# Performance work log

Measured on AMD Instinct MI355X. Metric: run time of the kernel, lower is better.

The kernel has to match this reference:

```python
import jax, jax.numpy as jnp
import numpy as np

N_USERS = 100_000
N_ITEMS = 100_000
D = 64            # args.in_size == args.out_size (GraphConv has weight=None)
N_INTENTS = 128   # hardcoded in DCCF
HID = 128         # SemanticAttention hidden_size
N_UI_EDGES = 1_000_000
N_MP_EDGES = 500_000
N_MP = 2          # metapaths per node type
B = 4096
N_LAYERS = 2      # hardcoded in DCCF


def setup_inputs() -> dict:
    key = jax.random.key(0)
    ks = jax.random.split(key, 20)
    s = 0.1
    inp = {}
    inp['user_feat'] = jax.random.normal(ks[0], (N_USERS, D), jnp.float32) * s
    inp['item_feat'] = jax.random.normal(ks[1], (N_ITEMS, D), jnp.float32) * s
    inp['user_intent'] = jax.random.normal(ks[2], (D, N_INTENTS), jnp.float32) * s
    inp['item_intent'] = jax.random.normal(ks[3], (D, N_INTENTS), jnp.float32) * s
    inp['sa_u_W1'] = jax.random.normal(ks[4], (D, HID), jnp.float32) * s
    inp['sa_u_b1'] = jnp.zeros((HID,), jnp.float32)
    inp['sa_u_w2'] = jax.random.normal(ks[5], (HID,), jnp.float32) * s
    inp['sa_i_W1'] = jax.random.normal(ks[6], (D, HID), jnp.float32) * s
    inp['sa_i_b1'] = jnp.zeros((HID,), jnp.float32)
    inp['sa_i_w2'] = jax.random.normal(ks[7], (HID,), jnp.float32) * s
    inp['ui_src'] = jax.random.randint(ks[8], (N_UI_EDGES,), 0, N_USERS)
    inp['ui_dst'] = jax.random.randint(ks[9], (N_UI_EDGES,), 0, N_ITEMS)
    inp['mp_user'] = jax.random.randint(ks[10], (N_MP, 2, N_MP_EDGES), 0, N_USERS)
    inp['mp_item'] = jax.random.randint(ks[11], (N_MP, 2, N_MP_EDGES), 0, N_ITEMS)
    # indices drawn WITHOUT replacement so torch.unique(index) in ssl_loss is a no-op
    inp['user_idx'] = jax.random.choice(ks[12], N_USERS, (B,), replace=False)
    inp['item_idx'] = jax.random.choice(ks[13], N_ITEMS, (B,), replace=False)
    inp['neg_item_idx'] = jax.random.randint(ks[14], (B,), 0, N_ITEMS)
    return inp


def _forward(user_feat, item_feat, user_intent, item_intent,
             sa_u_W1, sa_u_b1, sa_u_w2, sa_i_W1, sa_i_b1, sa_i_w2,
             ui_src, ui_dst, mp_user, mp_item, user_idx, item_idx, neg_item_idx):
    n_nodes = N_USERS + N_ITEMS
    # symmetric bipartite adjacency in COO (tmp_adj + tmp_adj.T)
    rows = jnp.concatenate([ui_src, ui_dst + N_USERS])
    cols = jnp.concatenate([ui_dst + N_USERS, ui_src])
    deg = jnp.maximum(jax.ops.segment_sum(jnp.ones_like(rows, jnp.float32), rows,
                                          num_segments=n_nodes), 1.0)
    dinv = jax.lax.rsqrt(deg)
    gv = dinv[rows] * dinv[cols]  # G = D^{-1/2} A D^{-1/2}

    def spmm(x):  # gather-scale-scatter, the torch_sparse.spmm
        return jax.ops.segment_sum(gv[:, None] * x[cols], rows, num_segments=n_nodes)

    # ---- DCCF ----
    emb = jnp.concatenate([user_feat, item_feat], axis=0)
    total = emb
    for _ in range(N_LAYERS):
        gnn = spmm(emb)
        u, it = emb[:N_USERS], emb[N_USERS:]
        u_int = jax.nn.softmax(u @ user_intent, axis=1) @ user_intent.T
        i_int = jax.nn.softmax(it @ item_intent, axis=1) @ item_intent.T
        emb = gnn + jnp.concatenate([u_int, i_int], axis=0) + emb
        total = total + emb  # torch.stack(...).sum(dim=1)
    ua, ia = total[:N_USERS], total[N_USERS:]

    # ---- HANLayer: GraphConv(norm='both', weight=None) per metapath ----
    def graphconv(src, dst, h, n):
        ones = jnp.ones_like(src, jnp.float32)
        outdeg = jnp.maximum(jax.ops.segment_sum(ones, src, num_segments=n), 1.0)
        indeg = jnp.maximum(jax.ops.segment_sum(ones, dst, num_segments=n), 1.0)
        x = h * jax.lax.rsqrt(outdeg)[:, None]
        agg = jax.ops.segment_sum(x[src], dst, num_segments=n)
        return agg * jax.lax.rsqrt(indeg)[:, None]

    def sem_att(z, W1, b1, w2):  # z: [N, M, D]
        w = jnp.mean(jnp.tanh(z @ W1 + b1) @ w2, axis=0)  # [M]
        beta = jax.nn.softmax(w)
        return jnp.einsum('m,nmd->nd', beta, z)

    zu = jnp.stack([graphconv(mp_user[m, 0], mp_user[m, 1], user_feat, N_USERS)
                    for m in range(N_MP)], axis=1)
    h2_u = sem_att(zu, sa_u_W1, sa_u_b1, sa_u_w2)
    zi = jnp.stack([graphconv(mp_item[m, 0], mp_item[m, 1], item_feat, N_ITEMS)
                    for m in range(N_MP)], axis=1)
    h2_i = sem_att(zi, sa_i_W1, sa_i_b1, sa_i_w2)

    user_emb = 0.5 * ua + 0.5 * h2_u
    item_emb = 0.5 * ia + 0.5 * h2_i

    def ssl(d1, d2, idx):  # InfoNCE with temp 0.5 (idx already unique)
        e1 = d1[idx]
        e2 = d2[idx]
        e1 = e1 / jnp.linalg.norm(e1, axis=1, keepdims=True)
        e2 = e2 / jnp.linalg.norm(e2, axis=1, keepdims=True)
        pos = jnp.sum(e1 * e2, axis=1) / 0.5
        lse = jax.nn.logsumexp(e1 @ e2.T / 0.5, axis=1)
        return -jnp.sum(pos - lse) / idx.shape[0]

    ssl_loss = ssl(h2_u, ua, user_idx) + ssl(h2_i, ia, item_idx)
    return (user_emb[user_idx], item_emb[item_idx], item_emb[neg_item_idx], ssl_loss)


def reference(user_feat, item_feat, user_intent, item_intent,
              sa_u_W1, sa_u_b1, sa_u_w2, sa_i_W1, sa_i_b1, sa_i_w2,
              ui_src, ui_dst, mp_user, mp_item, user_idx, item_idx, neg_item_idx):
    return _forward(user_feat, item_feat, user_intent, item_intent,
                    sa_u_W1, sa_u_b1, sa_u_w2, sa_i_W1, sa_i_b1, sa_i_w2,
                    ui_src, ui_dst, mp_user, mp_item, user_idx, item_idx, neg_item_idx)
```

## Files before the change

### kernel.cpp

```cpp
#include <hip/hip_runtime.h>
#include <math.h>

#define NUSERS   100000
#define NITEMS   100000
#define NNODES   200000
#define DD       64
#define NI       128
#define E_UI     1000000
#define E_MP     500000
#define BB       4096
#define NSTRIP   6250

#define O_CNT       0LL
#define O_OUTCNT    600000LL
#define O_CURSOR    1000000LL
#define O_PARTIALS  1600000LL
#define O_UITB_U    1625600LL
#define O_UITB_I    1629696LL
#define O_UIB_U     1633792LL
#define O_UIB_I     1637888LL
#define O_W1B_U     1641984LL
#define O_W1B_I     1646080LL
#define O_SUMEXP    1700000LL
#define O_POS       1708192LL
#define ZEND        1716384LL
#define O_OFF       1716384LL
#define O_BSUM      2316448LL
#define O_DINV      2317472LL
#define O_OINV      2517472LL
#define O_IINV      2917472LL
#define O_ADJ       3317472LL
#define O_WSUM      7317472LL
#define O_EMBA      7317480LL
#define O_TOTAL     20117480LL
#define O_EMBB      32917480LL
#define O_E1U       45717480LL
#define O_E2U       45979624LL
#define O_E1I       46241768LL
#define O_E2I       46503912LL

typedef __attribute__((ext_vector_type(8))) short short8;
typedef __attribute__((ext_vector_type(4))) float f32x4;

__device__ __forceinline__ short f2bf(float x) {
  unsigned u = __float_as_uint(x);
  unsigned r = (u + 0x7FFFu + ((u >> 16) & 1u)) >> 16;
  return (short)r;
}

__global__ void k_hist_main(const int* __restrict__ src, const int* __restrict__ dst,
                            int* __restrict__ cnt) {
  int e = blockIdx.x * 256 + threadIdx.x;
  if (e < E_UI) {
    atomicAdd(&cnt[src[e]], 1);
    atomicAdd(&cnt[NUSERS + dst[e]], 1);
  }
}

__global__ void k_hist_mp(const int* __restrict__ mpu, const int* __restrict__ mpi,
                          int* __restrict__ cnt, int* __restrict__ outcnt) {
  int e = blockIdx.x * 256 + threadIdx.x;
  int g = blockIdx.y;
  if (e < E_MP) {
    const int* base = (g < 2) ? (mpu + (long long)g * 2 * E_MP)
                              : (mpi + (long long)(g - 2) * 2 * E_MP);
    int s = base[e];
    int d = base[E_MP + e];
    atomicAdd(&outcnt[g * NUSERS + s], 1);
    atomicAdd(&cnt[NNODES + g * NUSERS + d], 1);
  }
}

__global__ __launch_bounds__(1024) void k_scan1(const int* __restrict__ in, int* __restrict__ out,
                                                int* __restrict__ bsum, int n) {
  __shared__ int s[1024];
  int i = blockIdx.x * 1024 + threadIdx.x;
  int v = (i < n) ? in[i] : 0;
  s[threadIdx.x] = v;
  __syncthreads();
  for (int off = 1; off < 1024; off <<= 1) {
    int x = (threadIdx.x >= off) ? s[threadIdx.x - off] : 0;
    __syncthreads();
    s[threadIdx.x] += x;
    __syncthreads();
  }
  if (i < n) out[i] = s[threadIdx.x] - v;
  if (threadIdx.x == 1023) bsum[blockIdx.x] = s[1023];
}

__global__ __launch_bounds__(1024) void k_scan2(int* __restrict__ bsum, int nb) {
  __shared__ int s[1024];
  int v = (threadIdx.x < nb) ? bsum[threadIdx.x] : 0;
  s[threadIdx.x] = v;
  __syncthreads();
  for (int off = 1; off < 1024; off <<= 1) {
    int x = (threadIdx.x >= off) ? s[threadIdx.x - off] : 0;
    __syncthreads();
    s[threadIdx.x] += x;
    __syncthreads();
  }
  if (threadIdx.x < nb) bsum[threadIdx.x] = s[threadIdx.x] - v;
}

__global__ __launch_bounds__(1024) void k_scan3(int* __restrict__ out, const int* __restrict__ bsum, int n) {
  int i = blockIdx.x * 1024 + threadIdx.x;
  if (i < n) out[i] += bsum[blockIdx.x];
}

__global__ void k_inv(const int* __restrict__ cnt, const int* __restrict__ outcnt,
                      float* __restrict__ dinv, float* __restrict__ iinv, float* __restrict__ oinv) {
  int i = blockIdx.x * 256 + threadIdx.x;
  if (i < NNODES) {
    int c = cnt[i]; if (c < 1) c = 1;
    dinv[i] = 1.0f / sqrtf((float)c);
  } else if (i < 600000) {
    int c = cnt[i]; if (c < 1) c = 1;
    iinv[i - NNODES] = 1.0f / sqrtf((float)c);
  }
  if (i < 400000) {
    int c = outcnt[i]; if (c < 1) c = 1;
    oinv[i] = 1.0f / sqrtf((float)c);
  }
}

__global__ void k_scatter_main(const int* __restrict__ src, const int* __restrict__ dst,
                               const int* __restrict__ off, int* __restrict__ cursor,
                               int* __restrict__ adj) {
  int e = blockIdx.x * 256 + threadIdx.x;
  if (e < E_UI) {
    int u = src[e];
    int it = NUSERS + dst[e];
    int p = atomicAdd(&cursor[u], 1);
    adj[off[u] + p] = it;
    int q = atomicAdd(&cursor[it], 1);
    adj[off[it] + q] = u;
  }
}

__global__ void k_scatter_mp(const int* __restrict__ mpu, const int* __restrict__ mpi,
                             const int* __restrict__ off, int* __restrict__ cursor,
                             int* __restrict__ adj) {
  int e = blockIdx.x * 256 + threadIdx.x;
  int g = blockIdx.y;
  if (e < E_MP) {
    const int* base = (g < 2) ? (mpu + (long long)g * 2 * E_MP)
                              : (mpi + (long long)(g - 2) * 2 * E_MP);
    int s = base[e];
    int d = base[E_MP + e];
    int node = NNODES + g * NUSERS + d;
    int p = atomicAdd(&cursor[node], 1);
    adj[off[node] + p] = s;
  }
}

__global__ void k_init(const float4* __restrict__ uf, const float4* __restrict__ itf,
                       float4* __restrict__ emb) {
  int i = blockIdx.x * 256 + threadIdx.x;
  if (i < 3200000) {
    emb[i] = (i < 1600000) ? uf[i] : itf[i - 1600000];
  }
}

__global__ void k_tw(const float* __restrict__ UIu, const float* __restrict__ UIi,
                     const float* __restrict__ W1u, const float* __restrict__ W1i,
                     short* __restrict__ UITBu, short* __restrict__ UITBi,
                     short* __restrict__ UIBu,  short* __restrict__ UIBi,
                     short* __restrict__ W1Bu,  short* __restrict__ W1Bi) {
  int t = blockIdx.x * 256 + threadIdx.x;
  if (t < 8192) {
    int d = t >> 7, j = t & 127;
    UITBu[j * 64 + d] = f2bf(UIu[t]);
    UITBi[j * 64 + d] = f2bf(UIi[t]);
    UIBu[t] = f2bf(UIu[t]);
    UIBi[t] = f2bf(UIi[t]);
    W1Bu[j * 64 + d] = f2bf(W1u[t]);
    W1Bi[j * 64 + d] = f2bf(W1i[t]);
  }
}

__device__ __forceinline__ float gather_rows(const float* __restrict__ tbl,
                                             const int* __restrict__ adj,
                                             int start, int c,
                                             const float* __restrict__ warr, int wofs,
                                             int lane) {
  float acc = 0.0f;
  for (int kb = 0; kb < c; kb += 64) {
    int rem = c - kb; if (rem > 64) rem = 64;
    int mi = 0; float mw = 0.0f;
    if (lane < rem) { mi = adj[start + kb + lane]; mw = warr[wofs + mi]; }
    for (int k = 0; k < rem; k += 8) {
      int n0=__shfl(mi,k+0),n1=__shfl(mi,k+1),n2=__shfl(mi,k+2),n3=__shfl(mi,k+3);
      int n4=__shfl(mi,k+4),n5=__shfl(mi,k+5),n6=__shfl(mi,k+6),n7=__shfl(mi,k+7);
      float w0=__shfl(mw,k+0),w1=__shfl(mw,k+1),w2=__shfl(mw,k+2),w3=__shfl(mw,k+3);
      float w4=__shfl(mw,k+4),w5=__shfl(mw,k+5),w6=__shfl(mw,k+6),w7=__shfl(mw,k+7);
      float v0=tbl[((long long)n0<<6)+lane], v1=tbl[((long long)n1<<6)+lane];
      float v2=tbl[((long long)n2<<6)+lane], v3=tbl[((long long)n3<<6)+lane];
      float v4=tbl[((long long)n4<<6)+lane], v5=tbl[((long long)n5<<6)+lane];
      float v6=tbl[((long long)n6<<6)+lane], v7=tbl[((long long)n7<<6)+lane];
      acc += w0*v0; acc += w1*v1; acc += w2*v2; acc += w3*v3;
      acc += w4*v4; acc += w5*v5; acc += w6*v6; acc += w7*v7;
    }
  }
  return acc;
}

__global__ __launch_bounds__(256) void k_layer(
    const float* __restrict__ ecur, float* __restrict__ enext, float* __restrict__ total,
    const int* __restrict__ adj, const int* __restrict__ off, const int* __restrict__ cnt,
    const float* __restrict__ dinv,
    const short* __restrict__ UITBu, const short* __restrict__ UITBi,
    const short* __restrict__ UIBu,  const short* __restrict__ UIBi, int layer) {
  __shared__ float sZ[4][16 * 68];
  __shared__ float sP[4][16 * 132];
  int w = threadIdx.x >> 6, lane = threadIdx.x & 63;
  int nb = blockIdx.x * 64 + w * 16;
  const short* UITB = (nb < NUSERS) ? UITBu : UITBi;
  const short* UIB  = (nb < NUSERS) ? UIBu  : UIBi;
  float* rowZ = sZ[w];
  float* rowP = sP[w];

  for (int m = 0; m < 16; m++) {
    int node = nb + m;
    float acc = gather_rows(ecur, adj, off[node], cnt[node], dinv, 0, lane);
    rowZ[m * 68 + lane] = dinv[node] * acc;
  }

  int quad = lane >> 4, mrow = lane & 15;
  const float* vrow = ecur + (((long long)(nb + mrow)) << 6) + quad * 8;
  float4 va0 = *(const float4*)(vrow);
  float4 va1 = *(const float4*)(vrow + 4);
  float4 vc0 = *(const float4*)(vrow + 32);
  float4 vc1 = *(const float4*)(vrow + 36);
  short8 a0 = { f2bf(va0.x), f2bf(va0.y), f2bf(va0.z), f2bf(va0.w),
                f2bf(va1.x), f2bf(va1.y), f2bf(va1.z), f2bf(va1.w) };
  short8 a1 = { f2bf(vc0.x), f2bf(vc0.y), f2bf(vc0.z), f2bf(vc0.w),
                f2bf(vc1.x), f2bf(vc1.y), f2bf(vc1.z), f2bf(vc1.w) };
  float den0 = 0.f, den1 = 0.f, den2 = 0.f, den3 = 0.f;
  float* pw = rowP + (quad * 4) * 132 + mrow;
#pragma unroll
  for (int jt = 0; jt < 8; jt++) {
    const short* wr = UITB + ((jt * 16 + mrow) << 6) + quad * 8;
    short8 b0 = *(const short8*)(wr);
    short8 bh = *(const short8*)(wr + 32);
    f32x4 acc = {0.f, 0.f, 0.f, 0.f};
    acc = __builtin_amdgcn_mfma_f32_16x16x32_bf16(a0, b0, acc, 0, 0, 0);
    acc = __builtin_amdgcn_mfma_f32_16x16x32_bf16(a1, bh, acc, 0, 0, 0);
    float e0 = __expf(acc[0]), e1 = __expf(acc[1]);
    float e2 = __expf(acc[2]), e3 = __expf(acc[3]);
    den0 += e0; den1 += e1; den2 += e2; den3 += e3;
    float* pj = pw + jt * 16;
    pj[0] = e0; pj[132] = e1; pj[264] = e2; pj[396] = e3;
  }
  for (int mask = 1; mask <= 8; mask <<= 1) {
    den0 += __shfl_xor(den0, mask); den1 += __shfl_xor(den1, mask);
    den2 += __shfl_xor(den2, mask); den3 += __shfl_xor(den3, mask);
  }
  float rd0 = 1.f / den0, rd1 = 1.f / den1, rd2 = 1.f / den2, rd3 = 1.f / den3;

#pragma unroll
  for (int dt = 0; dt < 4; dt++) {
    f32x4 acc = {0.f, 0.f, 0.f, 0.f};
#pragma unroll
    for (int c = 0; c < 4; c++) {
      const float* pr = rowP + mrow * 132 + c * 32 + quad * 8;
      float4 p0 = *(const float4*)(pr);
      float4 p1 = *(const float4*)(pr + 4);
      short8 af = { f2bf(p0.x), f2bf(p0.y), f2bf(p0.z), f2bf(p0.w),
                    f2bf(p1.x), f2bf(p1.y), f2bf(p1.z), f2bf(p1.w) };
      const short* br = UIB + ((dt * 16 + mrow) << 7) + c * 32 + quad * 8;
      short8 bf = *(const short8*)(br);
      acc = __builtin_amdgcn_mfma_f32_16x16x32_bf16(af, bf, acc, 0, 0, 0);
    }
    int d = dt * 16 + mrow;
#define COMB(r, rd)                                                            \
    { int node = nb + quad * 4 + r;                                            \
      long long base = (((long long)node) << 6) + d;                           \
      float o = acc[r] * rd;                                                   \
      float gn = rowZ[(quad * 4 + r) * 68 + d];                                \
      float vv = ecur[base];                                                   \
      float ne = gn + o + vv;                                                  \
      enext[base] = ne;                                                        \
      total[base] = (layer == 0) ? (vv + ne) : (total[base] + ne); }
    COMB(0, rd0) COMB(1, rd1) COMB(2, rd2) COMB(3, rd3)
#undef COMB
  }
}

__global__ __launch_bounds__(256, 6) void k_mp_gather(
    const float* __restrict__ uf, const float* __restrict__ itf,
    const int* __restrict__ adj, const int* __restrict__ off, const int* __restrict__ cnt,
    const float* __restrict__ oinv, const float* __restrict__ iinv,
    float* __restrict__ zu, float* __restrict__ zi) {
  int g = blockIdx.y;
  const float* feat = (g < 2) ? uf : itf;
  float* zb = (g < 2) ? zu + ((long long)g * NUSERS << 6)
                      : zi + ((long long)(g - 2) * NUSERS << 6);
  int n = (blockIdx.x << 2) + (threadIdx.x >> 6);
  int lane = threadIdx.x & 63;
  int gofs = g * NUSERS;
  int node = NNODES + gofs + n;
  float z = gather_rows(feat, adj, off[node], cnt[node], oinv, gofs, lane);
  zb[((long long)n << 6) + lane] = z * iinv[gofs + n];
}

__global__ __launch_bounds__(256, 4) void k_mp_mlp(
    const float* __restrict__ zu, const float* __restrict__ zi,
    const short* __restrict__ W1Bu, const float* __restrict__ b1u, const float* __restrict__ w2u,
    const short* __restrict__ W1Bi, const float* __restrict__ b1i, const float* __restrict__ w2i,
    float* __restrict__ partials) {
  int g = blockIdx.y;
  const short* W1B = (g < 2) ? W1Bu : W1Bi;
  const float* b1  = (g < 2) ? b1u : b1i;
  const float* w2  = (g < 2) ? w2u : w2i;
  const float* zb  = (g < 2) ? zu + ((long long)g * NUSERS << 6)
                             : zi + ((long long)(g - 2) * NUSERS << 6);
  int w = threadIdx.x >> 6, lane = threadIdx.x & 63;
  int strip = blockIdx.x * 4 + w;
  if (strip >= NSTRIP) return;
  int quad = lane >> 4, mrow = lane & 15;
  const float* zrow = zb + (((long long)(strip * 16 + mrow)) << 6) + quad * 8;
  float4 za0 = *(const float4*)(zrow);
  float4 za1 = *(const float4*)(zrow + 4);
  float4 zc0 = *(const float4*)(zrow + 32);
  float4 zc1 = *(const float4*)(zrow + 36);
  short8 a0 = { f2bf(za0.x), f2bf(za0.y), f2bf(za0.z), f2bf(za0.w),
                f2bf(za1.x), f2bf(za1.y), f2bf(za1.z), f2bf(za1.w) };
  short8 a1 = { f2bf(zc0.x), f2bf(zc0.y), f2bf(zc0.z), f2bf(zc0.w),
                f2bf(zc1.x), f2bf(zc1.y), f2bf(zc1.z), f2bf(zc1.w) };
  float psum = 0.0f;
#pragma unroll
  for (int jt = 0; jt < 8; jt++) {
    const short* wr = W1B + ((jt * 16 + mrow) << 6) + quad * 8;
    short8 b0 = *(const short8*)(wr);
    short8 bh = *(const short8*)(wr + 32);
    f32x4 acc = {0.f, 0.f, 0.f, 0.f};
    acc = __builtin_amdgcn_mfma_f32_16x16x32_bf16(a0, b0, acc, 0, 0, 0);
    acc = __builtin_amdgcn_mfma_f32_16x16x32_bf16(a1, bh, acc, 0, 0, 0);
    int j = jt * 16 + mrow;
    float bj = b1[j], wj = w2[j];
#pragma unroll
    for (int r = 0; r < 4; r++) {
      float s = acc[r] + bj;
      psum += wj * (1.0f - 2.0f / (__expf(2.0f * s) + 1.0f));
    }
  }
  for (int m = 32; m; m >>= 1) psum += __shfl_xor(psum, m);
  if (lane == 0) partials[g * NSTRIP + strip] = psum;
}

__global__ void k_beta(const float* __restrict__ partials, float* __restrict__ wsum) {
  int g = blockIdx.x;
  float s = 0.0f;
  for (int i = threadIdx.x; i < NSTRIP; i += 256) s += partials[g * NSTRIP + i];
  for (int m = 32; m; m >>= 1) s += __shfl_xor(s, m);
  __shared__ float r[4];
  if ((threadIdx.x & 63) == 0) r[threadIdx.x >> 6] = s;
  __syncthreads();
  if (threadIdx.x == 0) wsum[g] = r[0] + r[1] + r[2] + r[3];
}

__global__ __launch_bounds__(256) void k_h2out(
    const float* __restrict__ zu, const float* __restrict__ zi,
    const int* __restrict__ user_idx, const int* __restrict__ item_idx, const int* __restrict__ neg_idx,
    const float* __restrict__ total,
    const float* __restrict__ wsum, float* __restrict__ out,
    float* __restrict__ e1u, float* __restrict__ e2u,
    float* __restrict__ e1i, float* __restrict__ e2i, float* __restrict__ pos) {
  int lane = threadIdx.x & 63;
  int row = (blockIdx.x << 2) + (threadIdx.x >> 6);
  int seg = row >> 12;
  int r = row & 4095;
  int idx;
  const float* zb;
  int gbase;
  if (seg == 0)      { idx = user_idx[r]; zb = zu; gbase = 0; }
  else if (seg == 1) { idx = item_idx[r]; zb = zi; gbase = 2; }
  else               { idx = neg_idx[r];  zb = zi; gbase = 2; }
  int tnode = gbase ? (NUSERS + idx) : idx;
  float t = total[((long long)tnode << 6) + lane];
  float w0 = wsum[gbase] * (1.0f / 100000.0f);
  float w1 = wsum[gbase + 1] * (1.0f / 100000.0f);
  float mb = fmaxf(w0, w1);
  float b0 = expf(w0 - mb), b1 = expf(w1 - mb);
  float bs = b0 + b1;
  b0 /= bs; b1 /= bs;
  float z0 = zb[((long long)idx << 6) + lane];
  float z1 = zb[(((long long)NUSERS + idx) << 6) + lane];
  float h2 = b0 * z0 + b1 * z1;
  out[((long long)row << 6) + lane] = 0.5f * t + 0.5f * h2;
  if (seg < 2) {
    float n1 = h2 * h2, n2 = t * t;
    for (int m = 32; m; m >>= 1) { n1 += __shfl_xor(n1, m); n2 += __shfl_xor(n2, m); }
    n1 = sqrtf(n1); n2 = sqrtf(n2);
    float a = h2 / n1, b = t / n2;
    float d = a * b;
    for (int m = 32; m; m >>= 1) d += __shfl_xor(d, m);
    float* e1 = seg ? e1i : e1u;
    float* e2 = seg ? e2i : e2u;
    e1[((long long)r << 6) + lane] = a;
    e2[((long long)r << 6) + lane] = b;
    if (lane == 0) pos[seg * BB + r] = 2.0f * d;
  }
}

__global__ __launch_bounds__(256) void k_gemm(const float* __restrict__ e1u, const float* __restrict__ e2u,
                                              const float* __restrict__ e1i, const float* __restrict__ e2i,
                                              float* __restrict__ sumexp) {
  int side = blockIdx.z;
  const float* A = side ? e1i : e1u;
  const float* Bm = side ? e2i : e2u;
  __shared__ float sA[64][68], sB[64][68];
  int bb = blockIdx.y, kk = blockIdx.x;
  int tid = threadIdx.x;
  for (int i = tid; i < 1024; i += 256) {
    int row = i >> 4, d4 = (i & 15) << 2;
    float4 a = *(const float4*)&A[(((long long)(bb * 64 + row)) << 6) + d4];
    float4 b = *(const float4*)&Bm[(((long long)(kk * 64 + row)) << 6) + d4];
    *(float4*)&sA[row][d4] = a;
    *(float4*)&sB[row][d4] = b;
  }
  __syncthreads();
  int tx = tid & 15, ty = tid >> 4;
  int r0 = ty << 2, c0 = tx << 2;
  float acc[4][4] = {{0}};
  for (int k = 0; k < 64; k += 4) {
    float4 a0 = *(const float4*)&sA[r0 + 0][k];
    float4 a1 = *(const float4*)&sA[r0 + 1][k];
    float4 a2 = *(const float4*)&sA[r0 + 2][k];
    float4 a3 = *(const float4*)&sA[r0 + 3][k];
    float4 b0 = *(const float4*)&sB[c0 + 0][k];
    float4 b1 = *(const float4*)&sB[c0 + 1][k];
    float4 b2 = *(const float4*)&sB[c0 + 2][k];
    float4 b3 = *(const float4*)&sB[c0 + 3][k];
#define DOT(u_, v_) (u_.x*v_.x + u_.y*v_.y + u_.z*v_.z + u_.w*v_.w)
    acc[0][0] += DOT(a0, b0); acc[0][1] += DOT(a0, b1); acc[0][2] += DOT(a0, b2); acc[0][3] += DOT(a0, b3);
    acc[1][0] += DOT(a1, b0); acc[1][1] += DOT(a1, b1); acc[1][2] += DOT(a1, b2); acc[1][3] += DOT(a1, b3);
    acc[2][0] += DOT(a2, b0); acc[2][1] += DOT(a2, b1); acc[2][2] += DOT(a2, b2); acc[2][3] += DOT(a2, b3);
    acc[3][0] += DOT(a3, b0); acc[3][1] += DOT(a3, b1); acc[3][2] += DOT(a3, b2); acc[3][3] += DOT(a3, b3);
#undef DOT
  }
#pragma unroll
  for (int i = 0; i < 4; i++) {
    float rs = __expf(2.0f * acc[i][0]) + __expf(2.0f * acc[i][1])
             + __expf(2.0f * acc[i][2]) + __expf(2.0f * acc[i][3]);
    for (int m = 1; m < 16; m <<= 1) rs += __shfl_xor(rs, m);
    if (tx == 0)
      __hip_atomic_fetch_add(&sumexp[side * BB + bb * 64 + r0 + i], rs,
                             __ATOMIC_RELAXED, __HIP_MEMORY_SCOPE_AGENT);
  }
}

__global__ void k_loss(const float* __restrict__ sumexp, const float* __restrict__ pos,
                       float* __restrict__ out) {
  float s = 0.0f;
  for (int i = threadIdx.x; i < 2 * BB; i += 256) s += logf(sumexp[i]) - pos[i];
  for (int m = 32; m; m >>= 1) s += __shfl_xor(s, m);
  __shared__ float r[4];
  if ((threadIdx.x & 63) == 0) r[threadIdx.x >> 6] = s;
  __syncthreads();
  if (threadIdx.x == 0) out[3 * BB * DD] = (r[0] + r[1] + r[2] + r[3]) * (1.0f / (float)BB);
}

extern "C" void kernel_launch(void* const* d_in, const int* in_sizes, int n_in,
                              void* d_out, int out_size, void* d_ws, size_t ws_size,
                              hipStream_t stream) {
  const float* uf  = (const float*)d_in[0];
  const float* itf = (const float*)d_in[1];
  const float* UIu = (const float*)d_in[2];
  const float* UIi = (const float*)d_in[3];
  const float* W1u = (const float*)d_in[4];
  const float* b1u = (const float*)d_in[5];
  const float* w2u = (const float*)d_in[6];
  const float* W1i = (const float*)d_in[7];
  const float* b1i = (const float*)d_in[8];
  const float* w2i = (const float*)d_in[9];
  const int* ui_src   = (const int*)d_in[10];
  const int* ui_dst   = (const int*)d_in[11];
  const int* mpu      = (const int*)d_in[12];
  const int* mpi      = (const int*)d_in[13];
  const int* user_idx = (const int*)d_in[14];
  const int* item_idx = (const int*)d_in[15];
  const int* neg_idx  = (const int*)d_in[16];
  float* out = (float*)d_out;

  float* wf = (float*)d_ws;
  int*   wi = (int*)d_ws;

  int*   cnt      = wi + O_CNT;
  int*   outcnt   = wi + O_OUTCNT;
  int*   cursor   = wi + O_CURSOR;
  float* partials = wf + O_PARTIALS;
  short* UITBu    = (short*)(wf + O_UITB_U);
  short* UITBi    = (short*)(wf + O_UITB_I);
  short* UIBu     = (short*)(wf + O_UIB_U);
  short* UIBi     = (short*)(wf + O_UIB_I);
  short* W1Bu     = (short*)(wf + O_W1B_U);
  short* W1Bi     = (short*)(wf + O_W1B_I);
  float* sumexp   = wf + O_SUMEXP;
  float* pos      = wf + O_POS;
  int*   off      = wi + O_OFF;
  int*   bsum     = wi + O_BSUM;
  float* dinv     = wf + O_DINV;
  float* oinv     = wf + O_OINV;
  float* iinv     = wf + O_IINV;
  int*   adj      = wi + O_ADJ;
  float* wsum     = wf + O_WSUM;
  float* emba     = wf + O_EMBA;
  float* total    = wf + O_TOTAL;
  float* embb     = wf + O_EMBB;
  float* e1u      = wf + O_E1U;
  float* e2u      = wf + O_E2U;
  float* e1i      = wf + O_E1I;
  float* e2i      = wf + O_E2I;

  hipMemsetAsync(d_ws, 0, (size_t)ZEND * 4, stream);

  k_hist_main<<<(E_UI + 255) / 256, 256, 0, stream>>>(ui_src, ui_dst, cnt);
  k_hist_mp<<<dim3((E_MP + 255) / 256, 4), 256, 0, stream>>>(mpu, mpi, cnt, outcnt);

  const int NSCAN = 600000;
  const int NB = (NSCAN + 1023) / 1024;
  k_scan1<<<NB, 1024, 0, stream>>>(cnt, off, bsum, NSCAN);
  k_scan2<<<1, 1024, 0, stream>>>(bsum, NB);
  k_scan3<<<NB, 1024, 0, stream>>>(off, bsum, NSCAN);

  k_inv<<<(600000 + 255) / 256, 256, 0, stream>>>(cnt, outcnt, dinv, iinv, oinv);

  k_scatter_main<<<(E_UI + 255) / 256, 256, 0, stream>>>(ui_src, ui_dst, off, cursor, adj);
  k_scatter_mp<<<dim3((E_MP + 255) / 256, 4), 256, 0, stream>>>(mpu, mpi, off, cursor, adj);

  k_init<<<(3200000 + 255) / 256, 256, 0, stream>>>((const float4*)uf, (const float4*)itf,
                                                    (float4*)emba);
  k_tw<<<32, 256, 0, stream>>>(UIu, UIi, W1u, W1i, UITBu, UITBi, UIBu, UIBi, W1Bu, W1Bi);

  k_layer<<<3125, 256, 0, stream>>>(emba, embb, total, adj, off, cnt, dinv,
                                    UITBu, UITBi, UIBu, UIBi, 0);
  k_layer<<<3125, 256, 0, stream>>>(embb, emba, total, adj, off, cnt, dinv,
                                    UITBu, UITBi, UIBu, UIBi, 1);

  k_mp_gather<<<dim3(25000, 4), 256, 0, stream>>>(uf, itf, adj, off, cnt, oinv, iinv,
                                                  emba, embb);
  k_mp_mlp<<<dim3((NSTRIP + 3) / 4, 4), 256, 0, stream>>>(emba, embb, W1Bu, b1u, w2u,
                                                          W1Bi, b1i, w2i, partials);
  k_beta<<<4, 256, 0, stream>>>(partials, wsum);

  k_h2out<<<3072, 256, 0, stream>>>(emba, embb, user_idx, item_idx, neg_idx, total,
                                    wsum, out, e1u, e2u, e1i, e2i, pos);

  k_gemm<<<dim3(64, 64, 2), 256, 0, stream>>>(e1u, e2u, e1i, e2i, sumexp);
  k_loss<<<1, 256, 0, stream>>>(sumexp, pos, out);
}
```

Before: 1.355 ms.

## Batch neighbor index loads across nodes and use readlane for gather broadcasts

The graph gather now loads offsets, counts, first-64 neighbor indices and weights for 8 nodes (layer kernel) or 4 nodes (metapath kernel) up front. This exposes more independent memory requests per wave instead of serializing latency node by node. Broadcasts use readlane (scalar) instead of shuffles, and the metapath kernel handles four nodes per wave with a quarter of the blocks. The softmax probabilities are stored as bf16 in shared memory rather than fp32, and the layer kernel gets a launch-bounds occupancy hint. The batching adds register pressure.

```diff
diff --git a/kernel.cpp b/kernel.cpp
--- a/kernel.cpp
+++ b/kernel.cpp
@@ -178,51 +178,89 @@
   }
 }
 
-__device__ __forceinline__ float gather_rows(const float* __restrict__ tbl,
+__device__ __forceinline__ float acc8(const float* __restrict__ tbl, int miv, float mwv,
+                                      int rem, int lane, float acc) {
+  unsigned wb = __float_as_uint(mwv);
+  for (int k = 0; k < rem; k += 8) {
+    int n0 = __builtin_amdgcn_readlane(miv, k + 0);
+    int n1 = __builtin_amdgcn_readlane(miv, k + 1);
+    int n2 = __builtin_amdgcn_readlane(miv, k + 2);
+    int n3 = __builtin_amdgcn_readlane(miv, k + 3);
+    int n4 = __builtin_amdgcn_readlane(miv, k + 4);
+    int n5 = __builtin_amdgcn_readlane(miv, k + 5);
+    int n6 = __builtin_amdgcn_readlane(miv, k + 6);
+    int n7 = __builtin_amdgcn_readlane(miv, k + 7);
+    float w0 = __uint_as_float(__builtin_amdgcn_readlane(wb, k + 0));
+    float w1 = __uint_as_float(__builtin_amdgcn_readlane(wb, k + 1));
+    float w2 = __uint_as_float(__builtin_amdgcn_readlane(wb, k + 2));
+    float w3 = __uint_as_float(__builtin_amdgcn_readlane(wb, k + 3));
+    float w4 = __uint_as_float(__builtin_amdgcn_readlane(wb, k + 4));
+    float w5 = __uint_as_float(__builtin_amdgcn_readlane(wb, k + 5));
+    float w6 = __uint_as_float(__builtin_amdgcn_readlane(wb, k + 6));
+    float w7 = __uint_as_float(__builtin_amdgcn_readlane(wb, k + 7));
+    float v0 = tbl[((long long)n0 << 6) + lane], v1 = tbl[((long long)n1 << 6) + lane];
+    float v2 = tbl[((long long)n2 << 6) + lane], v3 = tbl[((long long)n3 << 6) + lane];
+    float v4 = tbl[((long long)n4 << 6) + lane], v5 = tbl[((long long)n5 << 6) + lane];
+    float v6 = tbl[((long long)n6 << 6) + lane], v7 = tbl[((long long)n7 << 6) + lane];
+    acc += w0 * v0; acc += w1 * v1; acc += w2 * v2; acc += w3 * v3;
+    acc += w4 * v4; acc += w5 * v5; acc += w6 * v6; acc += w7 * v7;
+  }
+  return acc;
+}
+
+__device__ __forceinline__ float gather_tail(const float* __restrict__ tbl,
                                              const int* __restrict__ adj,
                                              int start, int c,
                                              const float* __restrict__ warr, int wofs,
-                                             int lane) {
-  float acc = 0.0f;
-  for (int kb = 0; kb < c; kb += 64) {
+                                             int lane, float acc) {
+  for (int kb = 64; kb < c; kb += 64) {
     int rem = c - kb; if (rem > 64) rem = 64;
-    int mi = 0; float mw = 0.0f;
-    if (lane < rem) { mi = adj[start + kb + lane]; mw = warr[wofs + mi]; }
-    for (int k = 0; k < rem; k += 8) {
-      int n0=__shfl(mi,k+0),n1=__shfl(mi,k+1),n2=__shfl(mi,k+2),n3=__shfl(mi,k+3);
-      int n4=__shfl(mi,k+4),n5=__shfl(mi,k+5),n6=__shfl(mi,k+6),n7=__shfl(mi,k+7);
-      float w0=__shfl(mw,k+0),w1=__shfl(mw,k+1),w2=__shfl(mw,k+2),w3=__shfl(mw,k+3);
-      float w4=__shfl(mw,k+4),w5=__shfl(mw,k+5),w6=__shfl(mw,k+6),w7=__shfl(mw,k+7);
-      float v0=tbl[((long long)n0<<6)+lane], v1=tbl[((long long)n1<<6)+lane];
-      float v2=tbl[((long long)n2<<6)+lane], v3=tbl[((long long)n3<<6)+lane];
-      float v4=tbl[((long long)n4<<6)+lane], v5=tbl[((long long)n5<<6)+lane];
-      float v6=tbl[((long long)n6<<6)+lane], v7=tbl[((long long)n7<<6)+lane];
-      acc += w0*v0; acc += w1*v1; acc += w2*v2; acc += w3*v3;
-      acc += w4*v4; acc += w5*v5; acc += w6*v6; acc += w7*v7;
-    }
+    int ti = 0; float tw = 0.0f;
+    if (lane < rem) { ti = adj[start + kb + lane]; tw = warr[wofs + ti]; }
+    acc = acc8(tbl, ti, tw, rem, lane, acc);
   }
   return acc;
 }
 
-__global__ __launch_bounds__(256) void k_layer(
+__global__ __launch_bounds__(256, 4) void k_layer(
     const float* __restrict__ ecur, float* __restrict__ enext, float* __restrict__ total,
     const int* __restrict__ adj, const int* __restrict__ off, const int* __restrict__ cnt,
     const float* __restrict__ dinv,
     const short* __restrict__ UITBu, const short* __restrict__ UITBi,
     const short* __restrict__ UIBu,  const short* __restrict__ UIBi, int layer) {
   __shared__ float sZ[4][16 * 68];
-  __shared__ float sP[4][16 * 132];
+  __shared__ short sP[4][16 * 136];
   int w = threadIdx.x >> 6, lane = threadIdx.x & 63;
   int nb = blockIdx.x * 64 + w * 16;
   const short* UITB = (nb < NUSERS) ? UITBu : UITBi;
   const short* UIB  = (nb < NUSERS) ? UIBu  : UIBi;
   float* rowZ = sZ[w];
-  float* rowP = sP[w];
-
-  for (int m = 0; m < 16; m++) {
-    int node = nb + m;
-    float acc = gather_rows(ecur, adj, off[node], cnt[node], dinv, 0, lane);
-    rowZ[m * 68 + lane] = dinv[node] * acc;
+  short* rowP = sP[w];
+
+#pragma unroll
+  for (int h = 0; h < 2; h++) {
+    int nb8 = nb + h * 8;
+    int ofs[8], cns[8];
+    int mi[8]; float mw[8];
+#pragma unroll
+    for (int m = 0; m < 8; m++) {
+      ofs[m] = __builtin_amdgcn_readfirstlane(off[nb8 + m]);
+      cns[m] = __builtin_amdgcn_readfirstlane(cnt[nb8 + m]);
+    }
+#pragma unroll
+    for (int m = 0; m < 8; m++)
+      mi[m] = (lane < cns[m]) ? adj[ofs[m] + lane] : 0;
+#pragma unroll
+    for (int m = 0; m < 8; m++)
+      mw[m] = (lane < cns[m]) ? dinv[mi[m]] : 0.0f;
+#pragma unroll
+    for (int m = 0; m < 8; m++) {
+      int c = cns[m];
+      int rem = c < 64 ? c : 64;
+      float acc = acc8(ecur, mi[m], mw[m], rem, lane, 0.0f);
+      if (c > 64) acc = gather_tail(ecur, adj, ofs[m], c, dinv, 0, lane, acc);
+      rowZ[(h * 8 + m) * 68 + lane] = dinv[nb8 + m] * acc;
+    }
   }
 
   int quad = lane >> 4, mrow = lane & 15;
@@ -236,7 +274,7 @@
   short8 a1 = { f2bf(vc0.x), f2bf(vc0.y), f2bf(vc0.z), f2bf(vc0.w),
                 f2bf(vc1.x), f2bf(vc1.y), f2bf(vc1.z), f2bf(vc1.w) };
   float den0 = 0.f, den1 = 0.f, den2 = 0.f, den3 = 0.f;
-  float* pw = rowP + (quad * 4) * 132 + mrow;
+  short* pw = rowP + (quad * 4) * 136 + mrow;
 #pragma unroll
   for (int jt = 0; jt < 8; jt++) {
     const short* wr = UITB + ((jt * 16 + mrow) << 6) + quad * 8;
@@ -248,8 +286,8 @@
     float e0 = __expf(acc[0]), e1 = __expf(acc[1]);
     float e2 = __expf(acc[2]), e3 = __expf(acc[3]);
     den0 += e0; den1 += e1; den2 += e2; den3 += e3;
-    float* pj = pw + jt * 16;
-    pj[0] = e0; pj[132] = e1; pj[264] = e2; pj[396] = e3;
+    short* pj = pw + jt * 16;
+    pj[0] = f2bf(e0); pj[136] = f2bf(e1); pj[272] = f2bf(e2); pj[408] = f2bf(e3);
   }
   for (int mask = 1; mask <= 8; mask <<= 1) {
     den0 += __shfl_xor(den0, mask); den1 += __shfl_xor(den1, mask);
@@ -262,11 +300,8 @@
     f32x4 acc = {0.f, 0.f, 0.f, 0.f};
 #pragma unroll
     for (int c = 0; c < 4; c++) {
-      const float* pr = rowP + mrow * 132 + c * 32 + quad * 8;
-      float4 p0 = *(const float4*)(pr);
-      float4 p1 = *(const float4*)(pr + 4);
-      short8 af = { f2bf(p0.x), f2bf(p0.y), f2bf(p0.z), f2bf(p0.w),
-                    f2bf(p1.x), f2bf(p1.y), f2bf(p1.z), f2bf(p1.w) };
+      const short* pr = rowP + mrow * 136 + c * 32 + quad * 8;
+      short8 af = *(const short8*)(pr);
       const short* br = UIB + ((dt * 16 + mrow) << 7) + c * 32 + quad * 8;
       short8 bf = *(const short8*)(br);
       acc = __builtin_amdgcn_mfma_f32_16x16x32_bf16(af, bf, acc, 0, 0, 0);
@@ -295,12 +330,31 @@
   const float* feat = (g < 2) ? uf : itf;
   float* zb = (g < 2) ? zu + ((long long)g * NUSERS << 6)
                       : zi + ((long long)(g - 2) * NUSERS << 6);
-  int n = (blockIdx.x << 2) + (threadIdx.x >> 6);
-  int lane = threadIdx.x & 63;
+  int w = threadIdx.x >> 6, lane = threadIdx.x & 63;
+  int n0 = (blockIdx.x * 4 + w) * 4;
   int gofs = g * NUSERS;
-  int node = NNODES + gofs + n;
-  float z = gather_rows(feat, adj, off[node], cnt[node], oinv, gofs, lane);
-  zb[((long long)n << 6) + lane] = z * iinv[gofs + n];
+  int ofs[4], cns[4];
+  int mi[4]; float mw[4];
+#pragma unroll
+  for (int m = 0; m < 4; m++) {
+    int node = NNODES + gofs + n0 + m;
+    ofs[m] = __builtin_amdgcn_readfirstlane(off[node]);
+    cns[m] = __builtin_amdgcn_readfirstlane(cnt[node]);
+  }
+#pragma unroll
+  for (int m = 0; m < 4; m++)
+    mi[m] = (lane < cns[m]) ? adj[ofs[m] + lane] : 0;
+#pragma unroll
+  for (int m = 0; m < 4; m++)
+    mw[m] = (lane < cns[m]) ? oinv[gofs + mi[m]] : 0.0f;
+#pragma unroll
+  for (int m = 0; m < 4; m++) {
+    int c = cns[m];
+    int rem = c < 64 ? c : 64;
+    float acc = acc8(feat, mi[m], mw[m], rem, lane, 0.0f);
+    if (c > 64) acc = gather_tail(feat, adj, ofs[m], c, oinv, gofs, lane, acc);
+    zb[((long long)(n0 + m) << 6) + lane] = acc * iinv[gofs + n0 + m];
+  }
 }
 
 __global__ __launch_bounds__(256, 4) void k_mp_mlp(
@@ -538,8 +592,8 @@
   k_layer<<<3125, 256, 0, stream>>>(embb, emba, total, adj, off, cnt, dinv,
                                     UITBu, UITBi, UIBu, UIBi, 1);
 
-  k_mp_gather<<<dim3(25000, 4), 256, 0, stream>>>(uf, itf, adj, off, cnt, oinv, iinv,
-                                                  emba, embb);
+  k_mp_gather<<<dim3(6250, 4), 256, 0, stream>>>(uf, itf, adj, off, cnt, oinv, iinv,
+                                                 emba, embb);
   k_mp_mlp<<<dim3((NSTRIP + 3) / 4, 4), 256, 0, stream>>>(emba, embb, W1Bu, b1u, w2u,
                                                           W1Bi, b1i, w2i, partials);
   k_beta<<<4, 256, 0, stream>>>(partials, wsum);
```

Result: faster. 1.249 ms (-7.8%).
